# Kernel optimization log

Measured on AMD Instinct MI355X. Metric: run time of the kernel, lower is better.

The kernel has to match this reference:

```python
import jax, jax.numpy as jnp
from jax import lax
import numpy as np

TAU_R = 1.0
TAU_W = 5.0
W_MIN, W_MAX = 0.0, 0.05


def setup_inputs() -> dict:
    key = jax.random.key(0)
    ks = jax.random.split(key, 7)
    B, n_kc, n_mbon, n_fbn, n_ext, T = 48, 800, 20, 60, 2, 121
    n_dan = n_mbon
    n_recur = n_mbon + n_fbn + n_dan
    dt = 0.5
    sqrt2 = np.sqrt(2.0)
    # W_recur built per original init: per-block std sqrt(1/(sqrt2 * n_group))
    W_mbon = jax.random.normal(ks[0], (n_recur, n_mbon)) * np.sqrt(1.0 / (sqrt2 * n_mbon))
    W_fbn = jax.random.normal(ks[1], (n_recur, n_fbn)) * np.sqrt(1.0 / (sqrt2 * n_fbn))
    W_dan = jax.random.normal(ks[2], (n_recur, n_dan)) * np.sqrt(1.0 / (sqrt2 * n_dan))
    W_recur = jnp.concatenate([W_mbon, W_fbn, W_dan], axis=1).astype(jnp.float32)
    W_readout = (jax.random.normal(ks[3], (1, n_mbon)) / np.sqrt(float(n_mbon))).astype(jnp.float32)
    bias = jnp.full((n_recur,), 0.1, jnp.float32)
    W_ext = jax.random.normal(ks[4], (n_fbn, n_ext), jnp.float32)
    # sparse binary odor activity (f_ones = 0.1)
    r_kc = (jax.random.uniform(ks[5], (B, n_kc, T)) < 0.1).astype(jnp.float32)
    r_ext = jax.random.normal(ks[6], (B, n_ext, T), jnp.float32)
    time = jnp.arange(T, dtype=jnp.float32) * dt
    W_kc0 = jnp.full((B, n_mbon, n_kc), W_MAX, jnp.float32)  # W_kc_mbon_0
    wt0 = jnp.full((B, n_mbon, n_kc), W_MAX, jnp.float32)
    return {"r_kc": r_kc, "r_ext": r_ext, "time": time, "W_kc0": W_kc0,
            "wt0": wt0, "W_recur": W_recur, "W_readout": W_readout,
            "bias": bias, "W_ext": W_ext, "n_batch": B}


def reference(r_kc, r_ext, time, W_kc0, wt0, W_recur, W_readout, bias, W_ext, n_batch):
    n_mbon, n_kc = W_kc0.shape[1], W_kc0.shape[2]
    n_fbn = W_ext.shape[0]
    n_recur = W_recur.shape[0]
    n_dan = n_recur - n_mbon - n_fbn
    dt = time[1] - time[0]
    # n_hop == 0: DAN -> MBON weights zeroed (no knockouts)
    Wr = W_recur.at[:n_mbon, -n_dan:].set(0.0)
    # initial state: 0.1 everywhere, MBONs at 0
    r0 = jnp.full((n_batch, n_recur), 0.1, W_recur.dtype).at[:, :n_mbon].set(0.0)
    readout0 = r0[:, :n_mbon] @ W_readout.T  # [B, 1]
    readout0 = readout0[:, 0]
    rb_kc0 = r_kc[:, :, 0]
    rb_dan0 = r0[:, -n_dan:]
    # time-major driving inputs for the T-1 update steps
    xs = (jnp.moveaxis(r_kc, 2, 0)[:-1], jnp.moveaxis(r_ext, 2, 0)[:-1])

    def step(carry, x):
        r, W, wt, rb_kc, rb_dan = carry
        rkc_t, rext_t = x
        I_mbon = jnp.einsum('bmk,bk->bm', W, rkc_t)          # KC -> MBON via plastic W
        I_fbn = rext_t @ W_ext.T                              # context -> FBN
        I_tot = (jnp.zeros_like(r)
                 .at[:, :n_mbon].set(I_mbon)
                 .at[:, n_mbon:n_mbon + n_fbn].set(I_fbn))
        Wr_prod = r @ Wr.T                                    # 'bsr,br->bs'
        r_new = r + (-r + jax.nn.relu(Wr_prod + bias + I_tot)) * (dt / TAU_R)
        r_dan = r_new[:, -n_dan:]
        # eligibility traces (updated BEFORE computing dw, per wt_update)
        rb_kc_new = rb_kc + (rkc_t - rb_kc) * (dt / TAU_W)
        rb_dan_new = rb_dan + (r_dan - rb_dan) * (dt / TAU_W)
        # LTP - LTD plasticity (Eq 4)
        dw = (jnp.einsum('bd,bk->bdk', rb_dan_new, rkc_t)
              - jnp.einsum('bd,bk->bdk', r_dan, rb_kc_new))
        wt_new = wt + dw * dt
        W_new = jnp.clip(W + (-W + wt_new) * (dt / TAU_W), W_MIN, W_MAX)
        ro = (r_new[:, :n_mbon] @ W_readout.T)[:, 0]
        return (r_new, W_new, wt_new, rb_kc_new, rb_dan_new), (r_new, W_new, wt_new, ro)

    _, (rs, Ws, wts, ros) = lax.scan(step, (r0, W_kc0, wt0, rb_kc0, rb_dan0), xs)
    r_all = jnp.concatenate([r0[None], rs], axis=0)           # [T, B, n_recur]
    W_all = jnp.concatenate([W_kc0[None], Ws], axis=0)        # [T, B, n_mbon, n_kc]
    wt_all = jnp.concatenate([wt0[None], wts], axis=0)        # [T, B, n_mbon, n_kc]
    ro_all = jnp.concatenate([readout0[None], ros], axis=0)   # [T, B]
    return r_all, W_all, wt_all, ro_all
```

## Files before the change

kernel.cpp:

```cpp
#include <hip/hip_runtime.h>


#define NB   48
#define NK   800
#define NM   20
#define NF   60
#define NE   2
#define TT   121
#define NR   100
#define ND   20
#define NSTEP 120

#define R_OFF   0
#define W_OFF   580800
#define WT_OFF  93508800
#define RO_OFF  186436800

__global__ __launch_bounds__(640)
void rnn_step_kernel(const float* __restrict__ r_kc,
                     const float* __restrict__ r_ext,
                     const float* __restrict__ timev,
                     const float* __restrict__ W_kc0,
                     const float* __restrict__ wt0,
                     const float* __restrict__ W_recur,
                     const float* __restrict__ W_readout,
                     const float* __restrict__ bias,
                     const float* __restrict__ W_ext,
                     float* __restrict__ out)
{
    const int b   = blockIdx.x;
    const int tid = threadIdx.x;
    const int d   = tid >> 5;
    const int kg  = tid & 31;

    __shared__ __align__(16) float Wr_sh[NR * NR];
    __shared__ __align__(16) float rkc_sh[NK];
    __shared__ __align__(16) float vsh[NK];
    __shared__ float rsh[NR];
    __shared__ float rnew_sh[NR];
    __shared__ float bias_sh[NR];
    __shared__ float Imbon_sh[NM];
    __shared__ float rbdan_sh[ND];
    __shared__ float rdan_sh[ND];
    __shared__ float Wro_sh[NM];

    const float dt  = timev[1] - timev[0];
    const float dtw = dt * 0.2f;
    const float dtr = dt;

    for (int idx = tid; idx < NR * NR; idx += 640) {
        int i = idx / NR, j = idx - i * NR;
        float w = W_recur[idx];
        if (i < NM && j >= NR - ND) w = 0.f;
        Wr_sh[idx] = w;
    }
    if (tid < NR) {
        bias_sh[tid] = bias[tid];
        float r0 = (tid < NM) ? 0.f : 0.1f;
        rsh[tid] = r0;
        out[R_OFF + (size_t)b * NR + tid] = r0;
    }
    if (tid < NM) { Wro_sh[tid] = W_readout[tid]; rbdan_sh[tid] = 0.1f; }
    if (tid == 0) out[RO_OFF + b] = 0.f;

    float4 Wv[7], wtv[7], uv[7];
    const size_t rowbase = ((size_t)b * NM + d) * NK;
    #pragma unroll
    for (int j = 0; j < 7; ++j) {
        int k0 = 4 * kg + 128 * j;
        if (k0 < NK) {
            Wv[j]  = *(const float4*)(W_kc0 + rowbase + k0);
            wtv[j] = *(const float4*)(wt0   + rowbase + k0);
            *(float4*)(out + W_OFF  + rowbase + k0) = Wv[j];
            *(float4*)(out + WT_OFF + rowbase + k0) = wtv[j];
        }
    }
    __syncthreads();

    for (int t = 0; t < NSTEP; ++t) {
        for (int k = tid; k < NK; k += 640) {
            float u = r_kc[((size_t)b * NK + k) * TT + t];
            rkc_sh[k] = u;
            float vold = (t == 0) ? u : vsh[k];
            vsh[k] = vold + (u - vold) * dtw;
        }
        __syncthreads();

        float partial = 0.f;
        #pragma unroll
        for (int j = 0; j < 7; ++j) {
            int k0 = 4 * kg + 128 * j;
            if (k0 < NK) {
                uv[j] = *(const float4*)&rkc_sh[k0];
                partial += Wv[j].x * uv[j].x + Wv[j].y * uv[j].y
                         + Wv[j].z * uv[j].z + Wv[j].w * uv[j].w;
            }
        }
        partial += __shfl_xor(partial, 1);
        partial += __shfl_xor(partial, 2);
        partial += __shfl_xor(partial, 4);
        partial += __shfl_xor(partial, 8);
        partial += __shfl_xor(partial, 16);
        if (kg == 0) Imbon_sh[d] = partial;

        float wp = 0.f;
        if (tid < 4 * NR) {
            int i = tid >> 2, jg = tid & 3;
            const float* wr = Wr_sh + i * NR + jg * 25;
            const float* rr = rsh + jg * 25;
            #pragma unroll
            for (int j = 0; j < 25; ++j) wp += rr[j] * wr[j];
            wp += __shfl_xor(wp, 1);
            wp += __shfl_xor(wp, 2);
        }
        __syncthreads();

        if (tid < 4 * NR && (tid & 3) == 0) {
            int i = tid >> 2;
            float Itot;
            if (i < NM) {
                Itot = Imbon_sh[i];
            } else if (i < NM + NF) {
                float e0 = r_ext[((size_t)b * NE + 0) * TT + t];
                float e1 = r_ext[((size_t)b * NE + 1) * TT + t];
                Itot = e0 * W_ext[(i - NM) * NE + 0] + e1 * W_ext[(i - NM) * NE + 1];
            } else {
                Itot = 0.f;
            }
            float act = fmaxf(wp + bias_sh[i] + Itot, 0.f);
            float rn  = rsh[i] + (act - rsh[i]) * dtr;
            rnew_sh[i] = rn;
            out[R_OFF + ((size_t)(t + 1) * NB + b) * NR + i] = rn;
        }
        __syncthreads();

        if (tid < ND) {
            float rd = rnew_sh[NR - ND + tid];
            rdan_sh[tid] = rd;
            rbdan_sh[tid] += (rd - rbdan_sh[tid]) * dtw;
        }
        if (tid >= 128 && tid < 128 + NR) rsh[tid - 128] = rnew_sh[tid - 128];
        if (tid == 64) {
            float ro = 0.f;
            #pragma unroll
            for (int m = 0; m < NM; ++m) ro += rnew_sh[m] * Wro_sh[m];
            out[RO_OFF + (size_t)(t + 1) * NB + b] = ro;
        }
        __syncthreads();

        float a = rbdan_sh[d];
        float c = rdan_sh[d];
        const size_t slab  = (size_t)(t + 1) * (NB * NM * NK);
        const size_t baseW  = W_OFF  + slab + rowbase;
        const size_t baseWT = WT_OFF + slab + rowbase;
        #pragma unroll
        for (int j = 0; j < 7; ++j) {
            int k0 = 4 * kg + 128 * j;
            if (k0 < NK) {
                float4 v4 = *(const float4*)&vsh[k0];
                wtv[j].x += dt * (a * uv[j].x - c * v4.x);
                wtv[j].y += dt * (a * uv[j].y - c * v4.y);
                wtv[j].z += dt * (a * uv[j].z - c * v4.z);
                wtv[j].w += dt * (a * uv[j].w - c * v4.w);
                Wv[j].x = fminf(fmaxf(Wv[j].x + (wtv[j].x - Wv[j].x) * dtw, 0.f), 0.05f);
                Wv[j].y = fminf(fmaxf(Wv[j].y + (wtv[j].y - Wv[j].y) * dtw, 0.f), 0.05f);
                Wv[j].z = fminf(fmaxf(Wv[j].z + (wtv[j].z - Wv[j].z) * dtw, 0.f), 0.05f);
                Wv[j].w = fminf(fmaxf(Wv[j].w + (wtv[j].w - Wv[j].w) * dtw, 0.f), 0.05f);
                *(float4*)(out + baseW  + k0) = Wv[j];
                *(float4*)(out + baseWT + k0) = wtv[j];
            }
        }
        __syncthreads();
    }
}

extern "C" void kernel_launch(void* const* d_in, const int* in_sizes, int n_in,
                              void* d_out, int out_size, void* d_ws, size_t ws_size,
                              hipStream_t stream) {
    const float* r_kc      = (const float*)d_in[0];
    const float* r_ext     = (const float*)d_in[1];
    const float* timev     = (const float*)d_in[2];
    const float* W_kc0     = (const float*)d_in[3];
    const float* wt0       = (const float*)d_in[4];
    const float* W_recur   = (const float*)d_in[5];
    const float* W_readout = (const float*)d_in[6];
    const float* bias      = (const float*)d_in[7];
    const float* W_ext     = (const float*)d_in[8];
    float* out = (float*)d_out;

    rnn_step_kernel<<<dim3(NB), dim3(640), 0, stream>>>(
        r_kc, r_ext, timev, W_kc0, wt0, W_recur, W_readout, bias, W_ext, out);
}
```

Baseline: 1.165 ms.

## Split plasticity weight writes into a separate wide-grid kernel

The recurrent dynamics kernel no longer writes the W and wt slabs. It still runs the weight recurrence on 48 blocks because the MBON input depends on W. A second kernel launched over B*NM blocks reads the DAN rates back from the output, recomputes the traces, and streams the large W/wt outputs with nontemporal stores. This spreads the store-heavy traffic across many more CUs, at the cost of duplicating the weight update math and adding a second launch.

```diff
diff --git a/kernel.cpp b/kernel.cpp
--- a/kernel.cpp
+++ b/kernel.cpp
@@ -10,23 +10,26 @@
 #define NR   100
 #define ND   20
 #define NSTEP 120
+#define SLAB (NB * NM * NK)
 
 #define R_OFF   0
 #define W_OFF   580800
 #define WT_OFF  93508800
 #define RO_OFF  186436800
 
+typedef float f4 __attribute__((ext_vector_type(4)));
+
 __global__ __launch_bounds__(640)
-void rnn_step_kernel(const float* __restrict__ r_kc,
-                     const float* __restrict__ r_ext,
-                     const float* __restrict__ timev,
-                     const float* __restrict__ W_kc0,
-                     const float* __restrict__ wt0,
-                     const float* __restrict__ W_recur,
-                     const float* __restrict__ W_readout,
-                     const float* __restrict__ bias,
-                     const float* __restrict__ W_ext,
-                     float* __restrict__ out)
+void rnn_dyn_kernel(const float* __restrict__ r_kc,
+                    const float* __restrict__ r_ext,
+                    const float* __restrict__ timev,
+                    const float* __restrict__ W_kc0,
+                    const float* __restrict__ wt0,
+                    const float* __restrict__ W_recur,
+                    const float* __restrict__ W_readout,
+                    const float* __restrict__ bias,
+                    const float* __restrict__ W_ext,
+                    float* __restrict__ out)
 {
     const int b   = blockIdx.x;
     const int tid = threadIdx.x;
@@ -71,8 +74,6 @@
         if (k0 < NK) {
             Wv[j]  = *(const float4*)(W_kc0 + rowbase + k0);
             wtv[j] = *(const float4*)(wt0   + rowbase + k0);
-            *(float4*)(out + W_OFF  + rowbase + k0) = Wv[j];
-            *(float4*)(out + WT_OFF + rowbase + k0) = wtv[j];
         }
     }
     __syncthreads();
@@ -150,9 +151,6 @@
 
         float a = rbdan_sh[d];
         float c = rdan_sh[d];
-        const size_t slab  = (size_t)(t + 1) * (NB * NM * NK);
-        const size_t baseW  = W_OFF  + slab + rowbase;
-        const size_t baseWT = WT_OFF + slab + rowbase;
         #pragma unroll
         for (int j = 0; j < 7; ++j) {
             int k0 = 4 * kg + 128 * j;
@@ -166,8 +164,89 @@
                 Wv[j].y = fminf(fmaxf(Wv[j].y + (wtv[j].y - Wv[j].y) * dtw, 0.f), 0.05f);
                 Wv[j].z = fminf(fmaxf(Wv[j].z + (wtv[j].z - Wv[j].z) * dtw, 0.f), 0.05f);
                 Wv[j].w = fminf(fmaxf(Wv[j].w + (wtv[j].w - Wv[j].w) * dtw, 0.f), 0.05f);
-                *(float4*)(out + baseW  + k0) = Wv[j];
-                *(float4*)(out + baseWT + k0) = wtv[j];
+            }
+        }
+        __syncthreads();
+    }
+}
+
+__global__ __launch_bounds__(256)
+void plasticity_kernel(const float* __restrict__ r_kc,
+                       const float* __restrict__ timev,
+                       const float* __restrict__ W_kc0,
+                       const float* __restrict__ wt0,
+                       float* out)
+{
+    const int bd  = blockIdx.x;
+    const int b   = bd / NM;
+    const int d   = bd - b * NM;
+    const int tid = threadIdx.x;
+
+    __shared__ float a_sh[NSTEP];
+    __shared__ float c_sh[NSTEP];
+    __shared__ __align__(16) float u_sh[8][NK + 4];
+
+    const float dt  = timev[1] - timev[0];
+    const float dtw = dt * 0.2f;
+
+    if (tid < NSTEP)
+        c_sh[tid] = out[R_OFF + ((size_t)(tid + 1) * NB + b) * NR + (NR - ND + d)];
+    __syncthreads();
+    if (tid == 0) {
+        float a = 0.1f;
+        for (int t = 0; t < NSTEP; ++t) { a += (c_sh[t] - a) * dtw; a_sh[t] = a; }
+    }
+
+    const size_t rowbase = ((size_t)b * NM + d) * NK;
+    const int  k0  = 4 * tid;
+    const bool act = (k0 < NK);
+    f4 Wv = {0.f, 0.f, 0.f, 0.f}, wtv = Wv, v4 = Wv;
+    if (act) {
+        Wv  = *(const f4*)(W_kc0 + rowbase + k0);
+        wtv = *(const f4*)(wt0   + rowbase + k0);
+        __builtin_nontemporal_store(Wv,  (f4*)(out + W_OFF  + rowbase + k0));
+        __builtin_nontemporal_store(wtv, (f4*)(out + WT_OFF + rowbase + k0));
+    }
+    __syncthreads();
+
+    const float* ub = r_kc + (size_t)b * NK * TT;
+
+    for (int ch = 0; ch < NSTEP / 8; ++ch) {
+        const int t0 = 8 * ch;
+        #pragma unroll
+        for (int it = 0; it < (NK * 8) / 256; ++it) {
+            int idx = tid + 256 * it;
+            int k = idx >> 3, tt = idx & 7;
+            u_sh[tt][k] = ub[(size_t)k * TT + t0 + tt];
+        }
+        __syncthreads();
+
+        if (act) {
+            #pragma unroll
+            for (int tt = 0; tt < 8; ++tt) {
+                const int t = t0 + tt;
+                f4 u4 = *(const f4*)&u_sh[tt][k0];
+                if (t == 0) {
+                    v4 = u4;
+                } else {
+                    v4.x += (u4.x - v4.x) * dtw;
+                    v4.y += (u4.y - v4.y) * dtw;
+                    v4.z += (u4.z - v4.z) * dtw;
+                    v4.w += (u4.w - v4.w) * dtw;
+                }
+                const float a = a_sh[t];
+                const float c = c_sh[t];
+                wtv.x += dt * (a * u4.x - c * v4.x);
+                wtv.y += dt * (a * u4.y - c * v4.y);
+                wtv.z += dt * (a * u4.z - c * v4.z);
+                wtv.w += dt * (a * u4.w - c * v4.w);
+                Wv.x = fminf(fmaxf(Wv.x + (wtv.x - Wv.x) * dtw, 0.f), 0.05f);
+                Wv.y = fminf(fmaxf(Wv.y + (wtv.y - Wv.y) * dtw, 0.f), 0.05f);
+                Wv.z = fminf(fmaxf(Wv.z + (wtv.z - Wv.z) * dtw, 0.f), 0.05f);
+                Wv.w = fminf(fmaxf(Wv.w + (wtv.w - Wv.w) * dtw, 0.f), 0.05f);
+                const size_t slab = (size_t)(t + 1) * SLAB;
+                __builtin_nontemporal_store(Wv,  (f4*)(out + W_OFF  + slab + rowbase + k0));
+                __builtin_nontemporal_store(wtv, (f4*)(out + WT_OFF + slab + rowbase + k0));
             }
         }
         __syncthreads();
@@ -188,6 +267,8 @@
     const float* W_ext     = (const float*)d_in[8];
     float* out = (float*)d_out;
 
-    rnn_step_kernel<<<dim3(NB), dim3(640), 0, stream>>>(
+    rnn_dyn_kernel<<<dim3(NB), dim3(640), 0, stream>>>(
         r_kc, r_ext, timev, W_kc0, wt0, W_recur, W_readout, bias, W_ext, out);
+    plasticity_kernel<<<dim3(NB * NM), dim3(256), 0, stream>>>(
+        r_kc, timev, W_kc0, wt0, out);
 }
```

Result: slower. 1.189 ms (+2.1%).
